# Optimization experiments

Measured on AMD Instinct MI355X. Metric: run time of the kernel, lower is better.

The kernel has to match this reference:

```python
import jax, jax.numpy as jnp
import numpy as np


def _avg_pool(x, s):
    # exact adaptive avg pool when H,W divisible by s == mean pooling k=stride=s
    if s == 1:
        return x
    B, C, H, W = x.shape
    return x.reshape(B, C, H // s, s, W // s, s).mean(axis=(3, 5))


def _attention(x):
    # q = x^T [B,N,C], k = x [B,C,N], v = x^T; attn = softmax(q@k); out = (attn@v)^T
    B, C, H, W = x.shape
    xf = x.reshape(B, C, H * W)                       # [B,C,N]
    scores = jnp.einsum('bcn,bcm->bnm', xf, xf)       # [B,N,N]
    attn = jax.nn.softmax(scores, axis=-1)
    out = jnp.einsum('bnm,bcm->bcn', attn, xf)        # [B,C,N]
    return out.reshape(B, C, H, W)


def setup_inputs() -> dict:
    key = jax.random.key(0)
    x = jax.random.normal(key, (4, 128, 64, 64), dtype=jnp.float32)
    return {"x": x}


def reference(x) -> jnp.ndarray:
    B, C, H, W = x.shape
    out = jnp.zeros_like(x)
    for scale in (4, 2, 1):
        block = _avg_pool(x, scale)
        block = _attention(block)
        # bilinear upsample, half-pixel centers == torch align_corners=False
        block = jax.image.resize(block, (B, C, H, W), method='bilinear')
        out = out + block
    return out
```

## Files before the change

### kernel.cpp

```cpp
#include <hip/hip_runtime.h>
#include <hip/hip_bf16.h>
#include <math.h>

typedef __attribute__((ext_vector_type(8))) short bf16x8;
typedef __attribute__((ext_vector_type(4))) float f32x4;

#define B_ 4
#define C_ 128
#define LOG2E 1.4426950408889634f

#define XT1_B   0ull
#define XTT1_B  4194304ull
#define O1P_B   8388608ull
#define ML1_B   25165824ull
#define TAIL_B  25690112ull
#define XT2_B   (TAIL_B + 0ull)
#define XTT2_B  (TAIL_B + 1048576ull)
#define XT4_B   (TAIL_B + 2097152ull)
#define XTT4_B  (TAIL_B + 2359296ull)
#define A2P_B   (TAIL_B + 2621440ull)
#define ML2_B   (TAIL_B + 11010048ull)
#define A4P_B   (TAIL_B + 11272192ull)
#define ML4_B   (TAIL_B + 11796480ull)
#define A2M_B   (TAIL_B + 11812864ull)
#define A4M_B   (TAIL_B + 12861440ull)

__device__ __forceinline__ float ex2(float x) { return __builtin_amdgcn_exp2f(x); }

__device__ __forceinline__ unsigned short f2bf(float f) {
    unsigned int u = __builtin_bit_cast(unsigned int, f);
    return (unsigned short)((u + 0x7FFFu + ((u >> 16) & 1u)) >> 16);
}
__device__ __forceinline__ float bf2f(unsigned short u) {
    unsigned int x = ((unsigned int)u) << 16;
    return __builtin_bit_cast(float, x);
}
__device__ __forceinline__ unsigned int pkbf(float lo, float hi) {
    union { __hip_bfloat162 h; unsigned int u; } c;
    c.h = __float22bfloat162_rn(make_float2(lo, hi));
    return c.u;
}
__device__ __forceinline__ void gload_lds16(const void* g, void* l) {
    __builtin_amdgcn_global_load_lds(
        (const __attribute__((address_space(1))) unsigned int*)g,
        (__attribute__((address_space(3))) unsigned int*)l, 16, 0, 0);
}

__global__ __launch_bounds__(256) void pool_all(const float* __restrict__ x,
                                                unsigned short* __restrict__ xt1,
                                                unsigned short* __restrict__ xtT1,
                                                unsigned short* __restrict__ xt2,
                                                unsigned short* __restrict__ xtT2,
                                                unsigned short* __restrict__ xt4,
                                                unsigned short* __restrict__ xtT4) {
    constexpr int RS = 257;
    __shared__ float lds[32 * RS];
    const int hp4 = blockIdx.x;
    const int c0  = blockIdx.y * 32;
    const int b   = blockIdx.z;
    const int t   = threadIdx.x;

    #pragma unroll
    for (int i = 0; i < 8; ++i) {
        int e4 = (i * 256 + t) * 4;
        int ci = e4 >> 8, rem = e4 & 255;
        float4 v = *reinterpret_cast<const float4*>(
            &x[((size_t)(b * C_ + c0 + ci) * 64 + (hp4 * 4 + (rem >> 6))) * 64 + (rem & 63)]);
        *reinterpret_cast<float4*>(&lds[ci * RS + rem]) = v;
    }
    __syncthreads();

    #pragma unroll
    for (int i = 0; i < 32; ++i) {
        int v = i * 256 + t;
        int ci = v & 31, pos = v >> 5;
        xt1[((size_t)b * 4096 + hp4 * 256 + pos) * C_ + c0 + ci] = f2bf(lds[ci * RS + pos]);
    }
    #pragma unroll
    for (int i = 0; i < 32; ++i) {
        int ci = i, pos = t;
        xtT1[((size_t)(b * C_ + c0 + ci)) * 4096 + hp4 * 256 + pos] = f2bf(lds[ci * RS + pos]);
    }
    #pragma unroll
    for (int i = 0; i < 8; ++i) {
        int v = i * 256 + t;
        int ci = v & 31, pz = v >> 5;
        int r2 = pz >> 5, w2 = pz & 31;
        float s = lds[ci * RS + (2*r2)*64 + 2*w2]     + lds[ci * RS + (2*r2)*64 + 2*w2 + 1]
                + lds[ci * RS + (2*r2+1)*64 + 2*w2]   + lds[ci * RS + (2*r2+1)*64 + 2*w2 + 1];
        xt2[((size_t)b * 1024 + (hp4*2 + r2)*32 + w2) * C_ + c0 + ci] = f2bf(s * 0.25f);
    }
    #pragma unroll
    for (int i = 0; i < 8; ++i) {
        int v = i * 256 + t;
        int pz = v & 63, ci = v >> 6;
        int r2 = pz >> 5, w2 = pz & 31;
        float s = lds[ci * RS + (2*r2)*64 + 2*w2]     + lds[ci * RS + (2*r2)*64 + 2*w2 + 1]
                + lds[ci * RS + (2*r2+1)*64 + 2*w2]   + lds[ci * RS + (2*r2+1)*64 + 2*w2 + 1];
        xtT2[((size_t)(b * C_ + c0 + ci)) * 1024 + (hp4*2 + r2)*32 + w2] = f2bf(s * 0.25f);
    }
    #pragma unroll
    for (int i = 0; i < 2; ++i) {
        int v = i * 256 + t;
        int ci = v & 31, w4 = v >> 5;
        float s = 0.f;
        #pragma unroll
        for (int r = 0; r < 4; ++r)
            #pragma unroll
            for (int j = 0; j < 4; ++j) s += lds[ci * RS + r*64 + w4*4 + j];
        xt4[((size_t)b * 256 + hp4*16 + w4) * C_ + c0 + ci] = f2bf(s * 0.0625f);
    }
    #pragma unroll
    for (int i = 0; i < 2; ++i) {
        int v = i * 256 + t;
        int w4 = v & 15, ci = v >> 4;
        float s = 0.f;
        #pragma unroll
        for (int r = 0; r < 4; ++r)
            #pragma unroll
            for (int j = 0; j < 4; ++j) s += lds[ci * RS + r*64 + w4*4 + j];
        xtT4[((size_t)(b * C_ + c0 + ci)) * 256 + hp4*16 + w4] = f2bf(s * 0.0625f);
    }
}

template<int N, int SPLIT>
__device__ __forceinline__ void attn_body(const unsigned short* __restrict__ xt,
                                          const unsigned short* __restrict__ xtT,
                                          unsigned short* __restrict__ op,
                                          float* __restrict__ ml,
                                          const int bid, char* lds) {
    constexpr int LOG2S = (SPLIT == 2) ? 1 : ((SPLIT == 4) ? 2 : 3);
    constexpr int QB = N / 128;
    constexpr int W2 = QB * SPLIT / 2;
    constexpr int NT = N / SPLIT / 64;
    static_assert(NT >= 2 && (NT & 1) == 0, "even NT >= 2 required");
    const int xcd   = bid & 7;
    const int b     = xcd >> 1;
    const int wi    = (xcd & 1) * W2 + (bid >> 3);
    const int split = wi & (SPLIT - 1);
    const int qx    = wi >> LOG2S;
    const int n0    = qx * 128;
    const int m_beg = split * (N / SPLIT);

    const int tid = threadIdx.x;
    const int w = tid >> 6, lane = tid & 63;
    const int g = lane >> 4, rho = lane & 15;

    const char* xb  = (const char*)(xt  + (size_t)b * N * C_);
    const char* xtb = (const char*)(xtT + (size_t)b * C_ * N);

    bf16x8 qf[2][4];
    #pragma unroll
    for (int tt = 0; tt < 2; ++tt) {
        const char* qr = xb + (size_t)(n0 + w * 32 + tt * 16 + rho) * 256;
        #pragma unroll
        for (int kc = 0; kc < 4; ++kc) {
            bf16x8 raw = *(const bf16x8*)(qr + kc * 64 + g * 16);
            bf16x8 s;
            #pragma unroll
            for (int e = 0; e < 8; ++e)
                s[e] = (short)f2bf(bf2f((unsigned short)raw[e]) * LOG2E);
            qf[tt][kc] = s;
        }
    }

    int kOff[4], vOff[4];
    #pragma unroll
    for (int k = 0; k < 4; ++k) {
        int D = (w * 4 + k) * 1024 + lane * 16;
        int row = D >> 8, colb = D & 255;
        kOff[k] = row * 256 + (colb ^ ((row & 15) << 4));
        int c = D >> 7, cb2 = D & 127;
        vOff[k] = c * (2 * N) + (cb2 ^ ((c & 7) << 4));
    }
    int qkOff[4][4], pvOff[8][2];
    #pragma unroll
    for (int mb = 0; mb < 4; ++mb) {
        int rowm = ((mb >> 1) << 5) + ((mb & 1) << 2) + ((rho >> 2) << 3) + (rho & 3);
        int swz = (rowm & 15) << 4;
        #pragma unroll
        for (int kc = 0; kc < 4; ++kc)
            qkOff[mb][kc] = rowm * 256 + ((kc * 64 + g * 16) ^ swz);
    }
    #pragma unroll
    for (int cb = 0; cb < 8; ++cb) {
        int c = cb * 16 + rho;
        int vswz = (c & 7) << 4;
        #pragma unroll
        for (int ks = 0; ks < 2; ++ks)
            pvOff[cb][ks] = c * 128 + ((ks * 64 + g * 16) ^ vswz);
    }

    char* const KB0 = lds;
    char* const KB1 = lds + 16384;
    char* const VB0 = lds + 32768;
    char* const VB1 = lds + 49152;
    const char* kG = xb  + (size_t)m_beg * 256;
    const char* vG = xtb + (size_t)m_beg * 2;

    auto stageK = [&](char* dst, int tile) {
        const char* s = kG + (size_t)tile * (64 * 256);
        #pragma unroll
        for (int k = 0; k < 4; ++k) gload_lds16(s + kOff[k], dst + (w * 4 + k) * 1024);
    };
    auto stageV = [&](char* dst, int tile) {
        const char* s = vG + (size_t)tile * (64 * 2);
        #pragma unroll
        for (int k = 0; k < 4; ++k) gload_lds16(s + vOff[k], dst + (w * 4 + k) * 1024);
    };

    f32x4 acc[2][8];
    #pragma unroll
    for (int tt = 0; tt < 2; ++tt)
        #pragma unroll
        for (int cb = 0; cb < 8; ++cb) acc[tt][cb] = (f32x4){0.f, 0.f, 0.f, 0.f};
    float m_run[2] = {-INFINITY, -INFINITY};
    float l_lane[2] = {0.f, 0.f};

    auto qkt = [&](const char* kb, f32x4 (&aS)[2][4]) {
        #pragma unroll
        for (int tt = 0; tt < 2; ++tt)
            #pragma unroll
            for (int mb = 0; mb < 4; ++mb) aS[tt][mb] = (f32x4){0.f, 0.f, 0.f, 0.f};
        #pragma unroll
        for (int mb = 0; mb < 4; ++mb)
            #pragma unroll
            for (int kc = 0; kc < 4; ++kc) {
                bf16x8 kf = *(const bf16x8*)(kb + qkOff[mb][kc]);
                aS[0][mb] = __builtin_amdgcn_mfma_f32_16x16x32_bf16(kf, qf[0][kc], aS[0][mb], 0, 0, 0);
                aS[1][mb] = __builtin_amdgcn_mfma_f32_16x16x32_bf16(kf, qf[1][kc], aS[1][mb], 0, 0, 0);
            }
    };

    auto smpv = [&](f32x4 (&aS)[2][4], const char* vb) {
        bf16x8 pb[2][2];
        #pragma unroll
        for (int tt = 0; tt < 2; ++tt) {
            float tm = aS[tt][0][0];
            #pragma unroll
            for (int mb = 0; mb < 4; ++mb)
                #pragma unroll
                for (int r = 0; r < 4; ++r) tm = fmaxf(tm, aS[tt][mb][r]);
            tm = fmaxf(tm, __shfl_xor(tm, 16));
            tm = fmaxf(tm, __shfl_xor(tm, 32));
            if (!__all(tm <= m_run[tt] + 6.0f)) {
                float nm = fmaxf(m_run[tt], tm);
                float sc = ex2(m_run[tt] - nm);
                l_lane[tt] *= sc;
                m_run[tt] = nm;
                #pragma unroll
                for (int cb = 0; cb < 8; ++cb) {
                    acc[tt][cb][0] *= sc; acc[tt][cb][1] *= sc;
                    acc[tt][cb][2] *= sc; acc[tt][cb][3] *= sc;
                }
            }
            float p[4][4];
            #pragma unroll
            for (int mb = 0; mb < 4; ++mb)
                #pragma unroll
                for (int r = 0; r < 4; ++r) {
                    p[mb][r] = ex2(aS[tt][mb][r] - m_run[tt]);
                    l_lane[tt] += p[mb][r];
                }
            #pragma unroll
            for (int ks = 0; ks < 2; ++ks) {
                union { bf16x8 v; unsigned int u[4]; } pk;
                pk.u[0] = pkbf(p[2 * ks][0],     p[2 * ks][1]);
                pk.u[1] = pkbf(p[2 * ks][2],     p[2 * ks][3]);
                pk.u[2] = pkbf(p[2 * ks + 1][0], p[2 * ks + 1][1]);
                pk.u[3] = pkbf(p[2 * ks + 1][2], p[2 * ks + 1][3]);
                pb[tt][ks] = pk.v;
            }
        }
        #pragma unroll
        for (int cb = 0; cb < 8; ++cb)
            #pragma unroll
            for (int ks = 0; ks < 2; ++ks) {
                bf16x8 vf = *(const bf16x8*)(vb + pvOff[cb][ks]);
                acc[0][cb] = __builtin_amdgcn_mfma_f32_16x16x32_bf16(vf, pb[0][ks], acc[0][cb], 0, 0, 0);
                acc[1][cb] = __builtin_amdgcn_mfma_f32_16x16x32_bf16(vf, pb[1][ks], acc[1][cb], 0, 0, 0);
            }
    };

    f32x4 accA[2][4], accB[2][4];

    stageK(KB0, 0); stageV(VB0, 0); stageK(KB1, 1); stageV(VB1, 1);
    asm volatile("s_waitcnt vmcnt(12)" ::: "memory");
    __builtin_amdgcn_s_barrier();
    qkt(KB0, accA);
    __builtin_amdgcn_s_barrier();
    if constexpr (NT > 2) stageK(KB0, 2);

    #pragma unroll 1
    for (int j = 0; j + 3 < NT; j += 2) {
        asm volatile("s_waitcnt vmcnt(8)" ::: "memory");
        __builtin_amdgcn_s_barrier();
        qkt(KB1, accB);
        smpv(accA, VB0);
        __builtin_amdgcn_s_barrier();
        stageK(KB1, j + 3);
        stageV(VB0, j + 2);
        asm volatile("s_waitcnt vmcnt(8)" ::: "memory");
        __builtin_amdgcn_s_barrier();
        qkt(KB0, accA);
        smpv(accB, VB1);
        __builtin_amdgcn_s_barrier();
        if (j + 4 < NT) stageK(KB0, j + 4);
        stageV(VB1, j + 3);
    }
    asm volatile("s_waitcnt vmcnt(4)" ::: "memory");
    __builtin_amdgcn_s_barrier();
    qkt(KB1, accB);
    smpv(accA, VB0);
    asm volatile("s_waitcnt vmcnt(0)" ::: "memory");
    __builtin_amdgcn_s_barrier();
    smpv(accB, VB1);

    #pragma unroll
    for (int tt = 0; tt < 2; ++tt) {
        l_lane[tt] += __shfl_xor(l_lane[tt], 16);
        l_lane[tt] += __shfl_xor(l_lane[tt], 32);
        const int n = n0 + w * 32 + tt * 16 + rho;
        #pragma unroll
        for (int cb = 0; cb < 8; ++cb)
            #pragma unroll
            for (int r = 0; r < 4; ++r)
                op[((size_t)(split * B_ + b) * C_ + cb * 16 + g * 4 + r) * N + n] = f2bf(acc[tt][cb][r]);
        if (g == 0) {
            ml[((size_t)(split * B_ + b) * N + n) * 2 + 0] = m_run[tt];
            ml[((size_t)(split * B_ + b) * N + n) * 2 + 1] = l_lane[tt];
        }
    }
}

__global__ __launch_bounds__(256, 2) void attn_fused(const unsigned short* __restrict__ xt1,
                                                     const unsigned short* __restrict__ xtT1,
                                                     unsigned short* __restrict__ o1p,
                                                     float* __restrict__ ml1,
                                                     const unsigned short* __restrict__ xt2,
                                                     const unsigned short* __restrict__ xtT2,
                                                     unsigned short* __restrict__ a2p,
                                                     float* __restrict__ ml2,
                                                     const unsigned short* __restrict__ xt4,
                                                     const unsigned short* __restrict__ xtT4,
                                                     unsigned short* __restrict__ a4p,
                                                     float* __restrict__ ml4) {
    __shared__ char lds[65536];
    const int bid = (int)blockIdx.x;
    if (bid < 256)
        attn_body<1024, 8>(xt2, xtT2, a2p, ml2, bid, lds);
    else if (bid < 272)
        attn_body<256, 2>(xt4, xtT4, a4p, ml4, bid - 256, lds);
    else
        attn_body<4096, 4>(xt1, xtT1, o1p, ml1, bid - 272, lds);
}

__global__ __launch_bounds__(256) void merge_small(const unsigned short* __restrict__ a2p,
                                                   const float* __restrict__ ml2,
                                                   const unsigned short* __restrict__ a4p,
                                                   const float* __restrict__ ml4,
                                                   unsigned short* __restrict__ a2m,
                                                   unsigned short* __restrict__ a4m) {
    int idx = blockIdx.x * 256 + threadIdx.x;
    if (idx < 4 * 128 * 1024) {
        int n = idx & 1023, c = (idx >> 10) & 127, b = idx >> 17;
        float M = -INFINITY;
        #pragma unroll
        for (int s = 0; s < 8; ++s) M = fmaxf(M, ml2[((s * 4 + b) * 1024 + n) * 2]);
        float L = 0.f, O = 0.f;
        #pragma unroll
        for (int s = 0; s < 8; ++s) {
            float wgt = ex2(ml2[((s * 4 + b) * 1024 + n) * 2] - M);
            L += ml2[((s * 4 + b) * 1024 + n) * 2 + 1] * wgt;
            O += bf2f(a2p[((size_t)((s * 4 + b) * 128 + c)) * 1024 + n]) * wgt;
        }
        a2m[((size_t)(b * 128 + c)) * 1024 + n] = f2bf(O / L);
    } else {
        int i2 = idx - 4 * 128 * 1024;
        if (i2 < 4 * 128 * 256) {
            int n = i2 & 255, c = (i2 >> 8) & 127, b = i2 >> 15;
            float M = fmaxf(ml4[((0 * 4 + b) * 256 + n) * 2], ml4[((1 * 4 + b) * 256 + n) * 2]);
            float L = 0.f, O = 0.f;
            #pragma unroll
            for (int s = 0; s < 2; ++s) {
                float wgt = ex2(ml4[((s * 4 + b) * 256 + n) * 2] - M);
                L += ml4[((s * 4 + b) * 256 + n) * 2 + 1] * wgt;
                O += bf2f(a4p[((size_t)((s * 4 + b) * 128 + c)) * 256 + n]) * wgt;
            }
            a4m[((size_t)(b * 128 + c)) * 256 + n] = f2bf(O / L);
        }
    }
}

template<int HS>
__device__ __forceinline__ float bilin(const unsigned short* __restrict__ a, int h, int w) {
    constexpr float sc = (float)HS / 64.0f;
    float sh = (h + 0.5f) * sc - 0.5f;
    float sw = (w + 0.5f) * sc - 0.5f;
    int h0 = (int)floorf(sh); float fh = sh - (float)h0;
    int w0 = (int)floorf(sw); float fw = sw - (float)w0;
    int h0c = max(h0, 0), h1c = min(h0 + 1, HS - 1);
    int w0c = max(w0, 0), w1c = min(w0 + 1, HS - 1);
    float v00 = bf2f(a[h0c * HS + w0c]), v01 = bf2f(a[h0c * HS + w1c]);
    float v10 = bf2f(a[h1c * HS + w0c]), v11 = bf2f(a[h1c * HS + w1c]);
    return (1.f - fh) * ((1.f - fw) * v00 + fw * v01)
         +        fh  * ((1.f - fw) * v10 + fw * v11);
}

__global__ __launch_bounds__(256) void combine_kernel(float* __restrict__ out,
                                                      const unsigned short* __restrict__ o1p,
                                                      const float* __restrict__ ml1,
                                                      const unsigned short* __restrict__ a2m,
                                                      const unsigned short* __restrict__ a4m) {
    int e = blockIdx.x * 256 + threadIdx.x;
    if (e >= B_ * C_ * 64 * 64) return;
    int w  = e & 63;
    int h  = (e >> 6) & 63;
    int bc = e >> 12;
    int b  = bc >> 7;
    int n  = (h << 6) | w;
    float M = -INFINITY;
    #pragma unroll
    for (int s = 0; s < 4; ++s) M = fmaxf(M, ml1[((size_t)(s * 4 + b) * 4096 + n) * 2]);
    float num = 0.f, den = 0.f;
    #pragma unroll
    for (int s = 0; s < 4; ++s) {
        float wgt = ex2(ml1[((size_t)(s * 4 + b) * 4096 + n) * 2] - M);
        den += ml1[((size_t)(s * 4 + b) * 4096 + n) * 2 + 1] * wgt;
        num += bf2f(o1p[((size_t)(s * 512 + bc)) * 4096 + n]) * wgt;
    }
    float v = num / den;
    v += bilin<32>(a2m + (size_t)bc * 1024, h, w);
    v += bilin<16>(a4m + (size_t)bc * 256,  h, w);
    out[e] = v;
}

extern "C" void kernel_launch(void* const* d_in, const int* in_sizes, int n_in,
                              void* d_out, int out_size, void* d_ws, size_t ws_size,
                              hipStream_t stream) {
    const float* x = (const float*)d_in[0];
    float* out = (float*)d_out;
    char* ws = (char*)d_ws;
    unsigned short* xt1  = (unsigned short*)(ws + XT1_B);
    unsigned short* xtT1 = (unsigned short*)(ws + XTT1_B);
    unsigned short* o1p  = (unsigned short*)(ws + O1P_B);
    float*          ml1  = (float*)(ws + ML1_B);
    unsigned short* xt2  = (unsigned short*)(ws + XT2_B);
    unsigned short* xtT2 = (unsigned short*)(ws + XTT2_B);
    unsigned short* xt4  = (unsigned short*)(ws + XT4_B);
    unsigned short* xtT4 = (unsigned short*)(ws + XTT4_B);
    unsigned short* a2p  = (unsigned short*)(ws + A2P_B);
    float*          ml2  = (float*)(ws + ML2_B);
    unsigned short* a4p  = (unsigned short*)(ws + A4P_B);
    float*          ml4  = (float*)(ws + ML4_B);
    unsigned short* a2m  = (unsigned short*)(ws + A2M_B);
    unsigned short* a4m  = (unsigned short*)(ws + A4M_B);

    pool_all<<<dim3(16, 4, B_), 256, 0, stream>>>(x, xt1, xtT1, xt2, xtT2, xt4, xtT4);
    attn_fused<<<784, 256, 0, stream>>>(xt1, xtT1, o1p, ml1,
                                        xt2, xtT2, a2p, ml2,
                                        xt4, xtT4, a4p, ml4);
    merge_small<<<2560, 256, 0, stream>>>(a2p, ml2, a4p, ml4, a2m, a4m);
    combine_kernel<<<(B_ * C_ * 64 * 64 + 255) / 256, 256, 0, stream>>>(out, o1p, ml1, a2m, a4m);
}
```

Before: 80.86 us.

## Fuse small-scale merge into combine and reduce scale-2 KV splits

Cuts the KV split count for the scale-2 attention from 8 to 2, which shrinks the grid from 784 to 592 blocks and the partial-output buffers. The separate merge_small kernel is removed: combine2 now runs one block per (batch, channel), merges the scale-2 and scale-4 partials into LDS, and does the bilinear upsampling from LDS. This drops one kernel launch and a global round trip. The pool kernel's transposed bf16 stores are also packed two per 32-bit write. In exchange, each scale-2 attention block does four times more work, which may lengthen the tail of the fused attention grid.

```diff
diff --git a/kernel.cpp b/kernel.cpp
--- a/kernel.cpp
+++ b/kernel.cpp
@@ -19,11 +19,9 @@
 #define XT4_B   (TAIL_B + 2097152ull)
 #define XTT4_B  (TAIL_B + 2359296ull)
 #define A2P_B   (TAIL_B + 2621440ull)
-#define ML2_B   (TAIL_B + 11010048ull)
-#define A4P_B   (TAIL_B + 11272192ull)
-#define ML4_B   (TAIL_B + 11796480ull)
-#define A2M_B   (TAIL_B + 11812864ull)
-#define A4M_B   (TAIL_B + 12861440ull)
+#define ML2_B   (TAIL_B + 4718592ull)
+#define A4P_B   (TAIL_B + 4784128ull)
+#define ML4_B   (TAIL_B + 5308416ull)
 
 __device__ __forceinline__ float ex2(float x) { return __builtin_amdgcn_exp2f(x); }
 
@@ -71,15 +69,22 @@
     __syncthreads();
 
     #pragma unroll
-    for (int i = 0; i < 32; ++i) {
-        int v = i * 256 + t;
-        int ci = v & 31, pos = v >> 5;
-        xt1[((size_t)b * 4096 + hp4 * 256 + pos) * C_ + c0 + ci] = f2bf(lds[ci * RS + pos]);
-    }
-    #pragma unroll
-    for (int i = 0; i < 32; ++i) {
-        int ci = i, pos = t;
-        xtT1[((size_t)(b * C_ + c0 + ci)) * 4096 + hp4 * 256 + pos] = f2bf(lds[ci * RS + pos]);
+    for (int i = 0; i < 16; ++i) {
+        int p  = i * 256 + t;
+        int c2 = p & 15;
+        int pos = p >> 4;
+        unsigned int v = pkbf(lds[(2 * c2) * RS + pos], lds[(2 * c2 + 1) * RS + pos]);
+        *reinterpret_cast<unsigned int*>(
+            &xt1[((size_t)b * 4096 + hp4 * 256 + pos) * C_ + c0 + 2 * c2]) = v;
+    }
+    #pragma unroll
+    for (int i = 0; i < 16; ++i) {
+        int p  = i * 256 + t;
+        int p2 = p & 127;
+        int ci = p >> 7;
+        unsigned int v = pkbf(lds[ci * RS + 2 * p2], lds[ci * RS + 2 * p2 + 1]);
+        *reinterpret_cast<unsigned int*>(
+            &xtT1[((size_t)(b * C_ + c0 + ci)) * 4096 + hp4 * 256 + 2 * p2]) = v;
     }
     #pragma unroll
     for (int i = 0; i < 8; ++i) {
@@ -347,92 +352,92 @@
                                                      float* __restrict__ ml4) {
     __shared__ char lds[65536];
     const int bid = (int)blockIdx.x;
-    if (bid < 256)
-        attn_body<1024, 8>(xt2, xtT2, a2p, ml2, bid, lds);
-    else if (bid < 272)
-        attn_body<256, 2>(xt4, xtT4, a4p, ml4, bid - 256, lds);
+    if (bid < 64)
+        attn_body<1024, 2>(xt2, xtT2, a2p, ml2, bid, lds);
+    else if (bid < 80)
+        attn_body<256, 2>(xt4, xtT4, a4p, ml4, bid - 64, lds);
     else
-        attn_body<4096, 4>(xt1, xtT1, o1p, ml1, bid - 272, lds);
-}
-
-__global__ __launch_bounds__(256) void merge_small(const unsigned short* __restrict__ a2p,
-                                                   const float* __restrict__ ml2,
-                                                   const unsigned short* __restrict__ a4p,
-                                                   const float* __restrict__ ml4,
-                                                   unsigned short* __restrict__ a2m,
-                                                   unsigned short* __restrict__ a4m) {
-    int idx = blockIdx.x * 256 + threadIdx.x;
-    if (idx < 4 * 128 * 1024) {
-        int n = idx & 1023, c = (idx >> 10) & 127, b = idx >> 17;
+        attn_body<4096, 4>(xt1, xtT1, o1p, ml1, bid - 80, lds);
+}
+
+__global__ __launch_bounds__(256) void combine2(float* __restrict__ out,
+                                                const unsigned short* __restrict__ o1p,
+                                                const float* __restrict__ ml1,
+                                                const unsigned short* __restrict__ a2p,
+                                                const float* __restrict__ ml2,
+                                                const unsigned short* __restrict__ a4p,
+                                                const float* __restrict__ ml4) {
+    __shared__ float a2s[1024];
+    __shared__ float a4s[256];
+    const int bc = (int)blockIdx.x;
+    const int b  = bc >> 7;
+    const int c  = bc & 127;
+    const int t  = threadIdx.x;
+
+    #pragma unroll
+    for (int i = 0; i < 4; ++i) {
+        int n = i * 256 + t;
+        float m0 = ml2[((0 * 4 + b) * 1024 + n) * 2], l0 = ml2[((0 * 4 + b) * 1024 + n) * 2 + 1];
+        float m1 = ml2[((1 * 4 + b) * 1024 + n) * 2], l1 = ml2[((1 * 4 + b) * 1024 + n) * 2 + 1];
+        float M  = fmaxf(m0, m1);
+        float w0 = ex2(m0 - M), w1 = ex2(m1 - M);
+        float O  = bf2f(a2p[((size_t)((0 * 4 + b) * 128 + c)) * 1024 + n]) * w0
+                 + bf2f(a2p[((size_t)((1 * 4 + b) * 128 + c)) * 1024 + n]) * w1;
+        a2s[n] = O / (l0 * w0 + l1 * w1);
+    }
+    {
+        int n = t;
+        float m0 = ml4[((0 * 4 + b) * 256 + n) * 2], l0 = ml4[((0 * 4 + b) * 256 + n) * 2 + 1];
+        float m1 = ml4[((1 * 4 + b) * 256 + n) * 2], l1 = ml4[((1 * 4 + b) * 256 + n) * 2 + 1];
+        float M  = fmaxf(m0, m1);
+        float w0 = ex2(m0 - M), w1 = ex2(m1 - M);
+        float O  = bf2f(a4p[((size_t)((0 * 4 + b) * 128 + c)) * 256 + n]) * w0
+                 + bf2f(a4p[((size_t)((1 * 4 + b) * 128 + c)) * 256 + n]) * w1;
+        a4s[n] = O / (l0 * w0 + l1 * w1);
+    }
+    __syncthreads();
+
+    #pragma unroll
+    for (int i = 0; i < 16; ++i) {
+        int e = i * 256 + t;
+        int h = e >> 6, w = e & 63;
         float M = -INFINITY;
         #pragma unroll
-        for (int s = 0; s < 8; ++s) M = fmaxf(M, ml2[((s * 4 + b) * 1024 + n) * 2]);
-        float L = 0.f, O = 0.f;
-        #pragma unroll
-        for (int s = 0; s < 8; ++s) {
-            float wgt = ex2(ml2[((s * 4 + b) * 1024 + n) * 2] - M);
-            L += ml2[((s * 4 + b) * 1024 + n) * 2 + 1] * wgt;
-            O += bf2f(a2p[((size_t)((s * 4 + b) * 128 + c)) * 1024 + n]) * wgt;
-        }
-        a2m[((size_t)(b * 128 + c)) * 1024 + n] = f2bf(O / L);
-    } else {
-        int i2 = idx - 4 * 128 * 1024;
-        if (i2 < 4 * 128 * 256) {
-            int n = i2 & 255, c = (i2 >> 8) & 127, b = i2 >> 15;
-            float M = fmaxf(ml4[((0 * 4 + b) * 256 + n) * 2], ml4[((1 * 4 + b) * 256 + n) * 2]);
-            float L = 0.f, O = 0.f;
-            #pragma unroll
-            for (int s = 0; s < 2; ++s) {
-                float wgt = ex2(ml4[((s * 4 + b) * 256 + n) * 2] - M);
-                L += ml4[((s * 4 + b) * 256 + n) * 2 + 1] * wgt;
-                O += bf2f(a4p[((size_t)((s * 4 + b) * 128 + c)) * 256 + n]) * wgt;
-            }
-            a4m[((size_t)(b * 128 + c)) * 256 + n] = f2bf(O / L);
-        }
-    }
-}
-
-template<int HS>
-__device__ __forceinline__ float bilin(const unsigned short* __restrict__ a, int h, int w) {
-    constexpr float sc = (float)HS / 64.0f;
-    float sh = (h + 0.5f) * sc - 0.5f;
-    float sw = (w + 0.5f) * sc - 0.5f;
-    int h0 = (int)floorf(sh); float fh = sh - (float)h0;
-    int w0 = (int)floorf(sw); float fw = sw - (float)w0;
-    int h0c = max(h0, 0), h1c = min(h0 + 1, HS - 1);
-    int w0c = max(w0, 0), w1c = min(w0 + 1, HS - 1);
-    float v00 = bf2f(a[h0c * HS + w0c]), v01 = bf2f(a[h0c * HS + w1c]);
-    float v10 = bf2f(a[h1c * HS + w0c]), v11 = bf2f(a[h1c * HS + w1c]);
-    return (1.f - fh) * ((1.f - fw) * v00 + fw * v01)
-         +        fh  * ((1.f - fw) * v10 + fw * v11);
-}
-
-__global__ __launch_bounds__(256) void combine_kernel(float* __restrict__ out,
-                                                      const unsigned short* __restrict__ o1p,
-                                                      const float* __restrict__ ml1,
-                                                      const unsigned short* __restrict__ a2m,
-                                                      const unsigned short* __restrict__ a4m) {
-    int e = blockIdx.x * 256 + threadIdx.x;
-    if (e >= B_ * C_ * 64 * 64) return;
-    int w  = e & 63;
-    int h  = (e >> 6) & 63;
-    int bc = e >> 12;
-    int b  = bc >> 7;
-    int n  = (h << 6) | w;
-    float M = -INFINITY;
-    #pragma unroll
-    for (int s = 0; s < 4; ++s) M = fmaxf(M, ml1[((size_t)(s * 4 + b) * 4096 + n) * 2]);
-    float num = 0.f, den = 0.f;
-    #pragma unroll
-    for (int s = 0; s < 4; ++s) {
-        float wgt = ex2(ml1[((size_t)(s * 4 + b) * 4096 + n) * 2] - M);
-        den += ml1[((size_t)(s * 4 + b) * 4096 + n) * 2 + 1] * wgt;
-        num += bf2f(o1p[((size_t)(s * 512 + bc)) * 4096 + n]) * wgt;
-    }
-    float v = num / den;
-    v += bilin<32>(a2m + (size_t)bc * 1024, h, w);
-    v += bilin<16>(a4m + (size_t)bc * 256,  h, w);
-    out[e] = v;
+        for (int s = 0; s < 4; ++s) M = fmaxf(M, ml1[((size_t)(s * 4 + b) * 4096 + e) * 2]);
+        float num = 0.f, den = 0.f;
+        #pragma unroll
+        for (int s = 0; s < 4; ++s) {
+            float wgt = ex2(ml1[((size_t)(s * 4 + b) * 4096 + e) * 2] - M);
+            den += ml1[((size_t)(s * 4 + b) * 4096 + e) * 2 + 1] * wgt;
+            num += bf2f(o1p[((size_t)(s * 512 + bc)) * 4096 + e]) * wgt;
+        }
+        float v = num / den;
+        {
+            float sh = (h + 0.5f) * 0.5f - 0.5f;
+            float sw = (w + 0.5f) * 0.5f - 0.5f;
+            int h0 = (int)floorf(sh); float fh = sh - (float)h0;
+            int w0 = (int)floorf(sw); float fw = sw - (float)w0;
+            int h0c = max(h0, 0), h1c = min(h0 + 1, 31);
+            int w0c = max(w0, 0), w1c = min(w0 + 1, 31);
+            float v00 = a2s[h0c * 32 + w0c], v01 = a2s[h0c * 32 + w1c];
+            float v10 = a2s[h1c * 32 + w0c], v11 = a2s[h1c * 32 + w1c];
+            v += (1.f - fh) * ((1.f - fw) * v00 + fw * v01)
+               +        fh  * ((1.f - fw) * v10 + fw * v11);
+        }
+        {
+            float sh = (h + 0.5f) * 0.25f - 0.5f;
+            float sw = (w + 0.5f) * 0.25f - 0.5f;
+            int h0 = (int)floorf(sh); float fh = sh - (float)h0;
+            int w0 = (int)floorf(sw); float fw = sw - (float)w0;
+            int h0c = max(h0, 0), h1c = min(h0 + 1, 15);
+            int w0c = max(w0, 0), w1c = min(w0 + 1, 15);
+            float v00 = a4s[h0c * 16 + w0c], v01 = a4s[h0c * 16 + w1c];
+            float v10 = a4s[h1c * 16 + w0c], v11 = a4s[h1c * 16 + w1c];
+            v += (1.f - fh) * ((1.f - fw) * v00 + fw * v01)
+               +        fh  * ((1.f - fw) * v10 + fw * v11);
+        }
+        out[(size_t)bc * 4096 + e] = v;
+    }
 }
 
 extern "C" void kernel_launch(void* const* d_in, const int* in_sizes, int n_in,
@@ -453,13 +458,10 @@
     float*          ml2  = (float*)(ws + ML2_B);
     unsigned short* a4p  = (unsigned short*)(ws + A4P_B);
     float*          ml4  = (float*)(ws + ML4_B);
-    unsigned short* a2m  = (unsigned short*)(ws + A2M_B);
-    unsigned short* a4m  = (unsigned short*)(ws + A4M_B);
 
     pool_all<<<dim3(16, 4, B_), 256, 0, stream>>>(x, xt1, xtT1, xt2, xtT2, xt4, xtT4);
-    attn_fused<<<784, 256, 0, stream>>>(xt1, xtT1, o1p, ml1,
+    attn_fused<<<592, 256, 0, stream>>>(xt1, xtT1, o1p, ml1,
                                         xt2, xtT2, a2p, ml2,
                                         xt4, xtT4, a4p, ml4);
-    merge_small<<<2560, 256, 0, stream>>>(a2p, ml2, a4p, ml4, a2m, a4m);
-    combine_kernel<<<(B_ * C_ * 64 * 64 + 255) / 256, 256, 0, stream>>>(out, o1p, ml1, a2m, a4m);
-}
+    combine2<<<512, 256, 0, stream>>>(out, o1p, ml1, a2p, ml2, a4p, ml4);
+}
```

Result: faster. 78.13 us (-3.4%).
